# Kernel optimization log

Measured on AMD Instinct MI355X. Metric: run time of the kernel, lower is better.

The kernel has to match this reference:

```python
import jax, jax.numpy as jnp
import numpy as np


def lstm(x, W, U, b):
    """Keras LSTM with activation='relu', recurrent_activation='sigmoid'.
    x: [B, S, E]; W: [E, 4u]; U: [u, 4u]; b: [4u]. Gate order i,f,c,o.
    Returns (all hidden states [B,S,u], last hidden [B,u])."""
    B = x.shape[0]
    u = U.shape[0]
    h0 = jnp.zeros((B, u), x.dtype)
    c0 = jnp.zeros((B, u), x.dtype)

    def step(carry, xt):
        h, c = carry
        z = xt @ W + h @ U + b
        i, f, g, o = jnp.split(z, 4, axis=-1)
        i = jax.nn.sigmoid(i)
        f = jax.nn.sigmoid(f)
        g = jax.nn.relu(g)          # candidate activation = relu
        o = jax.nn.sigmoid(o)
        c = f * c + i * g
        h = o * jax.nn.relu(c)      # output activation = relu
        return (h, c), h

    (hT, _), hs = jax.lax.scan(step, (h0, c0), jnp.swapaxes(x, 0, 1))
    return jnp.swapaxes(hs, 0, 1), hT


def setup_inputs() -> dict:
    key = jax.random.key(0)
    ks = iter(jax.random.split(key, 64))

    def W(*s):
        return jax.random.normal(next(ks), s, jnp.float32) * 0.05

    V = 32000
    inp = {
        "t": jax.random.randint(next(ks), (8, 16, 64), 0, V, jnp.int32),
        "p": jax.random.randint(next(ks), (8, 16, 512), 0, V, jnp.int32),
        "emb_t": W(V, 128),
        "emb_p": W(V, 256),
        # title LSTMs: 128 (return_seq) -> 64
        "tl0_W": W(128, 512), "tl0_U": W(128, 512), "tl0_b": jnp.zeros((512,), jnp.float32),
        "tl1_W": W(128, 256), "tl1_U": W(64, 256),  "tl1_b": jnp.zeros((256,), jnp.float32),
        # title dense: 128 relu, 64 relu, 32 linear
        "td0_W": W(64, 128),  "td0_b": jnp.zeros((128,), jnp.float32),
        "td1_W": W(128, 64),  "td1_b": jnp.zeros((64,), jnp.float32),
        "td2_W": W(64, 32),   "td2_b": jnp.zeros((32,), jnp.float32),
        # parag LSTMs: 256 (rs) -> 128 (rs) -> 64
        "pl0_W": W(256, 1024), "pl0_U": W(256, 1024), "pl0_b": jnp.zeros((1024,), jnp.float32),
        "pl1_W": W(256, 512),  "pl1_U": W(128, 512),  "pl1_b": jnp.zeros((512,), jnp.float32),
        "pl2_W": W(128, 256),  "pl2_U": W(64, 256),   "pl2_b": jnp.zeros((256,), jnp.float32),
        # parag dense: 128 relu, 64 relu, 32 linear
        "pd0_W": W(64, 128),  "pd0_b": jnp.zeros((128,), jnp.float32),
        "pd1_W": W(128, 64),  "pd1_b": jnp.zeros((64,), jnp.float32),
        "pd2_W": W(64, 32),   "pd2_b": jnp.zeros((32,), jnp.float32),
        # head: 256 relu, 128 relu, 64 relu, 32 sigmoid
        "L0_W": W(64, 256),  "L0_b": jnp.zeros((256,), jnp.float32),
        "L1_W": W(256, 128), "L1_b": jnp.zeros((128,), jnp.float32),
        "L2_W": W(128, 64),  "L2_b": jnp.zeros((64,), jnp.float32),
        "L3_W": W(64, 32),   "L3_b": jnp.zeros((32,), jnp.float32),
    }
    return inp


def reference(t, p, emb_t, emb_p,
              tl0_W, tl0_U, tl0_b, tl1_W, tl1_U, tl1_b,
              td0_W, td0_b, td1_W, td1_b, td2_W, td2_b,
              pl0_W, pl0_U, pl0_b, pl1_W, pl1_U, pl1_b, pl2_W, pl2_U, pl2_b,
              pd0_W, pd0_b, pd1_W, pd1_b, pd2_W, pd2_b,
              L0_W, L0_b, L1_W, L1_b, L2_W, L2_b, L3_W, L3_b):
    B, N, St = t.shape
    Sp = p.shape[2]

    # The original loops over B and map_fn over a singleton axis; the math is
    # identical to running the stacks on a flattened [B*N] recurrent batch.
    xt = emb_t[t.reshape(B * N, St)]              # [BN, St, 128]
    xt, _ = lstm(xt, tl0_W, tl0_U, tl0_b)         # [BN, St, 128]
    _, ht = lstm(xt, tl1_W, tl1_U, tl1_b)         # [BN, 64]
    ht = jax.nn.relu(ht @ td0_W + td0_b)
    ht = jax.nn.relu(ht @ td1_W + td1_b)
    ht = ht @ td2_W + td2_b                       # [BN, 32] (no activation)

    xp = emb_p[p.reshape(B * N, Sp)]              # [BN, Sp, 256]
    xp, _ = lstm(xp, pl0_W, pl0_U, pl0_b)
    xp, _ = lstm(xp, pl1_W, pl1_U, pl1_b)
    _, hp = lstm(xp, pl2_W, pl2_U, pl2_b)         # [BN, 64]
    hp = jax.nn.relu(hp @ pd0_W + pd0_b)
    hp = jax.nn.relu(hp @ pd1_W + pd1_b)
    hp = hp @ pd2_W + pd2_b                       # [BN, 32]

    feat = jnp.concatenate([ht, hp], axis=-1).reshape(B, N, 64)
    x = feat.mean(axis=1)                         # reduce_mean over axis=-2 (N)
    x = jax.nn.relu(x @ L0_W + L0_b)
    x = jax.nn.relu(x @ L1_W + L1_b)
    x = jax.nn.relu(x @ L2_W + L2_b)
    x = jax.nn.sigmoid(x @ L3_W + L3_b)           # [B, 32]
    return x
```

## Files before the change

kernel.cpp:

```cpp
#include <hip/hip_runtime.h>
#include <hip/hip_fp16.h>

typedef _Float16 f16;
typedef _Float16 f16x8 __attribute__((ext_vector_type(8)));
typedef float    f32x4 __attribute__((ext_vector_type(4)));
typedef unsigned short ushort;
typedef unsigned int uint;
typedef unsigned long long u64;

__device__ __forceinline__ float sigm(float x) { return 1.f / (1.f + __expf(-x)); }
__device__ __forceinline__ float reluf(float x) { return x > 0.f ? x : 0.f; }
__device__ __forceinline__ float h2f(ushort u) { return (float)__builtin_bit_cast(f16, u); }
__device__ __forceinline__ ushort f2h(float v) { return __builtin_bit_cast(ushort, (f16)v); }

#define LDRLX(p)    __hip_atomic_load((p), __ATOMIC_RELAXED, __HIP_MEMORY_SCOPE_AGENT)
#define STRLX(p, v) __hip_atomic_store((p), (v), __ATOMIC_RELAXED, __HIP_MEMORY_SCOPE_AGENT)
#define MFMA16(a, b, c) __builtin_amdgcn_mfma_f32_16x16x32_f16((a), (b), (c), 0, 0, 0)

__device__ __forceinline__ void poll_all(uint* p, uint need, bool act) {
  bool done = !act;
  while (true) {
    if (!done) done = (LDRLX(p) >= need);
    if (__all((int)done)) break;
    __builtin_amdgcn_s_sleep(1);
  }
}

__device__ __forceinline__ u64 ldr64(const u64* p) {
  return __hip_atomic_load(p, __ATOMIC_RELAXED, __HIP_MEMORY_SCOPE_AGENT);
}
__device__ __forceinline__ void str64(u64* p, u64 v) {
  __hip_atomic_store(p, v, __ATOMIC_RELAXED, __HIP_MEMORY_SCOPE_AGENT);
}

template <int NR>
__device__ __forceinline__ void poll_recs(const u64* const (&ra)[NR],
                                          const uint (&nd)[NR], u64 (&rv)[NR]) {
  bool ok[NR];
#pragma unroll
  for (int i = 0; i < NR; i++) ok[i] = (nd[i] == 0u);
  while (true) {
    bool all = true;
#pragma unroll
    for (int i = 0; i < NR; i++) if (!ok[i]) rv[i] = ldr64(ra[i]);
#pragma unroll
    for (int i = 0; i < NR; i++) if (!ok[i]) ok[i] = ((uint)(rv[i] >> 32) >= nd[i]);
#pragma unroll
    for (int i = 0; i < NR; i++) all &= ok[i];
    if (all) return;
    __builtin_amdgcn_s_sleep(1);
  }
}

template <int KF>
__global__ void pack_bsw(const float* __restrict__ B, f16* __restrict__ dst, int N) {
  int id = blockIdx.x * 256 + threadIdx.x;
  int total = KF * 32 * N;
  if (id >= total) return;
  int j  = id & 7;
  int L  = (id >> 3) & 63;
  int r  = id >> 9;
  int kf = r & (KF - 1);
  int c  = r / KF;
  int k  = kf * 32 + ((L >> 4) * 8) + j;
  int n  = c * 16 + (L & 15);
  dst[id] = (f16)B[k * N + n];
}

template <int Sx, int K, int KF, int N, int NC, int MODE>
__global__ __launch_bounds__(256) void gemm_xw(const int* __restrict__ tok,
                                               const float* __restrict__ emb,
                                               const f16* __restrict__ Bsw,
                                               const float* __restrict__ bias,
                                               f16* __restrict__ X) {
  __shared__ int tokLds[64];
  __shared__ f16x8 bLds[8 * 64];
  const int tid = threadIdx.x;
  const int blk = blockIdx.x;
  const int g  = (MODE == 0) ? (blk >> 7) : (blk >> 4);
  const int t0 = (MODE == 0) ? ((blk & 127) * 4) : ((blk & 15) * 4);
  if (tid < 64) {
    int wv = tid >> 4, rho = tid & 15;
    tokLds[tid] = tok[(g * 16 + rho) * Sx + t0 + wv];
  }
  __syncthreads();
  const int wave = tid >> 6, lane = tid & 63;
  const int quad = lane >> 4, l16 = lane & 15;

  f16x8 a[KF];
  {
    const float* arow = emb + (long)tokLds[wave * 16 + l16] * K + quad * 8;
#pragma unroll
    for (int kf = 0; kf < KF; kf++) {
      float4 v0 = *(const float4*)(arow + kf * 32);
      float4 v1 = *(const float4*)(arow + kf * 32 + 4);
      f16x8 tv;
      tv[0] = (f16)v0.x; tv[1] = (f16)v0.y; tv[2] = (f16)v0.z; tv[3] = (f16)v0.w;
      tv[4] = (f16)v1.x; tv[5] = (f16)v1.y; tv[6] = (f16)v1.z; tv[7] = (f16)v1.w;
      a[kf] = tv;
    }
  }
  const int t = t0 + wave;
  const f16x8* Bfrag = (const f16x8*)Bsw;
  for (int c = 0; c < NC; c++) {
    for (int i = tid; i < KF * 64; i += 256) bLds[i] = Bfrag[c * KF * 64 + i];
    __syncthreads();
    f32x4 acc = {0.f, 0.f, 0.f, 0.f};
#pragma unroll
    for (int kf = 0; kf < KF; kf++)
      acc = MFMA16(a[kf], bLds[kf * 64 + lane], acc);
    const int col = c * 16 + l16;
    const float bc = bias[col];
    uint2 pk;
    pk.x = (uint)f2h(acc[0] + bc) | ((uint)f2h(acc[1] + bc) << 16);
    pk.y = (uint)f2h(acc[2] + bc) | ((uint)f2h(acc[3] + bc) << 16);
    size_t base;
    if (MODE == 0) {
      int gm = col >> 8, u = col & 255;
      base = (((size_t)(g * 512 + t) * 4 + gm) * 4096) + u * 16 + quad * 4;
    } else {
      int gm = col >> 7, u = col & 127;
      base = (((size_t)(g * 64 + t) * 4 + gm) * 2048) + u * 16 + quad * 4;
    }
    *(uint2*)(X + base) = pk;
    __syncthreads();
  }
}

struct RP {
  const f16 *xp2, *xt2;
  const f16 *U0f, *W1f, *U1f, *W2f, *U2f, *U0tf, *W1tf, *U1tf;
  const float *pl1_b, *pl2_b, *tl1_b;
  const float *pd0W, *pd0b, *pd1W, *pd1b, *pd2W, *pd2b;
  const float *td0W, *td0b, *td1W, *td1b, *td2W, *td2b;
  u64 *h0r, *h1r, *h0tr;
  uint *cnt;
  float* feat;
};

__global__ __launch_bounds__(256, 1) void recur_pipe(RP A) {
  __shared__ __align__(16) char smem[147968];
  const int tid = threadIdx.x;
  const int w = tid >> 6, lane = tid & 63;
  const int quad = lane >> 4, l16 = lane & 15;
  const int blk = blockIdx.x;
  const int role = blk >> 3, g = blk & 7;
  uint* mytag = A.cnt + (role * 8 + g) * 16;

  if (role < 4) {
    const int bb = role;
    f16* wlds = (f16*)smem;
    f16* hb   = (f16*)(smem + 131072);
    {
      const uint4* U0q = (const uint4*)A.U0f;
      uint4* wq = (uint4*)wlds;
      for (int idx = tid; idx < 8192; idx += 256) {
        int gm = idx >> 11, r = idx & 2047, wv = r >> 9, kf = (r >> 6) & 7, ln = r & 63;
        wq[idx] = U0q[((gm * 16 + 4 * bb + wv) * 8 + kf) * 64 + ln];
      }
    }
    for (int idx = tid; idx < 4224; idx += 256) hb[idx] = (f16)0.f;
    float c0[4] = {0.f, 0.f, 0.f, 0.f};
    u64* ringg = A.h0r + (size_t)g * 16384;
    int pp[3]; { int q = 0; for (int p = 0; p < 4; p++) if (p != bb) pp[q++] = p; }
    const uint2* xq2 = (const uint2*)A.xp2;
    const f16x8* wv8 = (const f16x8*)wlds;
    const int myu = 64 * bb + 16 * w + l16;
    uint* bpp = A.cnt;
    if (lane < 4) bpp = A.cnt + ((4 + lane) * 8 + g) * 16;
    __syncthreads();

    for (int t = 0; t < 512; t++) {
      uint2 xv[4];
      {
        size_t xb = ((size_t)(g * 512 + t) * 4) * 1024 + (size_t)myu * 4 + quad;
#pragma unroll
        for (int gm = 0; gm < 4; gm++) xv[gm] = xq2[xb + (size_t)gm * 1024];
      }
      {
        bool act = (lane < 4) && (t > 0) && ((t & 3) == 0);
        uint need = t > 4 ? (uint)(t - 4) : 0u;
        poll_all(bpp, need, act);
      }
      {
        const u64* slotb = ringg + (size_t)((t + 7) & 7) * 2048;
        const u64* ra[6]; uint nd[6]; u64 rv[6];
#pragma unroll
        for (int q = 0; q < 3; q++) {
          const u64* rb = slotb + pp[q] * 512 + 2 * tid;
          ra[q * 2] = rb; ra[q * 2 + 1] = rb + 1;
          nd[q * 2] = nd[q * 2 + 1] = (t > 0) ? (uint)t : 0u;
        }
        poll_recs<6>(ra, nd, rv);
        if (t > 0) {
          f16* dst = hb + (t & 1) * 4224;
          const int ul = tid >> 2;
#pragma unroll
          for (int q = 0; q < 3; q++)
#pragma unroll
            for (int j = 0; j < 2; j++) {
              uint pay = (uint)rv[q * 2 + j];
              int r0 = ((tid & 3) * 2 + j) * 2;
              dst[r0 * 264 + pp[q] * 64 + ul] = __builtin_bit_cast(f16, (ushort)pay);
              dst[(r0 + 1) * 264 + pp[q] * 64 + ul] = __builtin_bit_cast(f16, (ushort)(pay >> 16));
            }
        }
      }
      __syncthreads();
      f16x8 af[8];
#pragma unroll
      for (int kf = 0; kf < 8; kf++)
        af[kf] = *(const f16x8*)&hb[(t & 1) * 4224 + l16 * 264 + kf * 32 + quad * 8];
      f32x4 z[4];
#pragma unroll
      for (int gm = 0; gm < 4; gm++) {
        f32x4 zz = {0.f, 0.f, 0.f, 0.f};
#pragma unroll
        for (int kf = 0; kf < 8; kf++)
          zz = MFMA16(af[kf], wv8[((gm * 4 + w) * 8 + kf) * 64 + lane], zz);
        z[gm] = zz;
      }
      u64 xs[4];
#pragma unroll
      for (int gm = 0; gm < 4; gm++) xs[gm] = ((u64)xv[gm].y << 32) | xv[gm].x;
      ushort hs[4];
      f16* wbuf = hb + ((t + 1) & 1) * 4224;
#pragma unroll
      for (int r = 0; r < 4; r++) {
        float gi = sigm(z[0][r] + h2f((ushort)(xs[0] >> (16 * r))));
        float ff = sigm(z[1][r] + h2f((ushort)(xs[1] >> (16 * r))));
        float gg = reluf(z[2][r] + h2f((ushort)(xs[2] >> (16 * r))));
        float oo = sigm(z[3][r] + h2f((ushort)(xs[3] >> (16 * r))));
        c0[r] = ff * c0[r] + gi * gg;
        hs[r] = f2h(oo * reluf(c0[r]));
        wbuf[(quad * 4 + r) * 264 + myu] = __builtin_bit_cast(f16, hs[r]);
      }
      {
        u64 tg = ((u64)(uint)(t + 1)) << 32;
        u64* wb = ringg + (size_t)(t & 7) * 2048 + bb * 512 + (16 * w + l16) * 8 + quad * 2;
        str64(wb,     tg | (u64)((uint)hs[0] | ((uint)hs[1] << 16)));
        str64(wb + 1, tg | (u64)((uint)hs[2] | ((uint)hs[3] << 16)));
      }
    }
  } else if (role < 8) {
    const int bn = role - 4;
    f16* wlds = (f16*)smem;
    f16* h0c  = (f16*)(smem + 98304);
    f16* h1b  = (f16*)(smem + 106752);
    float* zL = (float*)(smem + 115456);
    {
      const uint4* W1q = (const uint4*)A.W1f;
      const uint4* U1q = (const uint4*)A.U1f;
      uint4* wq = (uint4*)wlds;
      for (int idx = tid; idx < 4096; idx += 256) {
        int gm = idx >> 10, r = idx & 1023, j2 = r >> 9, kf = (r >> 6) & 7, ln = r & 63;
        wq[idx] = W1q[((gm * 8 + bn * 2 + j2) * 8 + kf) * 64 + ln];
      }
      for (int idx = tid; idx < 2048; idx += 256) {
        int gm = idx >> 9, r = idx & 511, j2 = r >> 8, kf = (r >> 6) & 3, ln = r & 63;
        wq[4096 + idx] = U1q[((gm * 8 + bn * 2 + j2) * 4 + kf) * 64 + ln];
      }
    }
    for (int idx = tid; idx < 2176; idx += 256) h1b[idx] = (f16)0.f;
    float c1[2] = {0.f, 0.f};
    float bth[4];
    { int un = tid & 31; for (int gm = 0; gm < 4; gm++) bth[gm] = A.pl1_b[gm * 128 + 32 * bn + un]; }
    u64* h0rg = A.h0r + (size_t)g * 16384;
    u64* h1rg = A.h1r + (size_t)g * 8192;
    int pp[3]; { int q = 0; for (int p = 0; p < 4; p++) if (p != bn) pp[q++] = p; }
    const f16x8* wv8 = (const f16x8*)wlds;
    uint* bpp = A.cnt + (8 * 8 + g) * 16;
    __syncthreads();

    for (int t = 0; t < 512; t++) {
      {
        bool act = (lane == 0) && ((t & 3) == 0);
        uint need = t > 4 ? (uint)(t - 4) : 0u;
        poll_all(bpp, need, act);
      }
      const u64* ra[11]; uint nd[11]; u64 rv[11];
      {
        const u64* s0b = h0rg + (size_t)(t & 7) * 2048;
#pragma unroll
        for (int e = 0; e < 8; e++) { ra[e] = s0b + tid + 256 * e; nd[e] = (uint)(t + 1); }
        const u64* s1b = h1rg + (size_t)((t + 7) & 7) * 1024;
#pragma unroll
        for (int q = 0; q < 3; q++) { ra[8 + q] = s1b + pp[q] * 256 + tid; nd[8 + q] = (t > 0) ? (uint)t : 0u; }
      }
      poll_recs<11>(ra, nd, rv);
      {
#pragma unroll
        for (int e = 0; e < 8; e++) {
          int idx = tid + 256 * e;
          int q = idx >> 9, rr = idx & 511, uls = rr >> 3, rp = rr & 7;
          uint pay = (uint)rv[e];
          h0c[(2 * rp) * 264 + q * 64 + uls]     = __builtin_bit_cast(f16, (ushort)pay);
          h0c[(2 * rp + 1) * 264 + q * 64 + uls] = __builtin_bit_cast(f16, (ushort)(pay >> 16));
        }
        if (t > 0) {
          f16* dst = h1b + (t & 1) * 2176;
          int un = tid >> 3, sq = tid & 7;
#pragma unroll
          for (int q = 0; q < 3; q++) {
            uint pay = (uint)rv[8 + q];
            dst[sq * 136 + pp[q] * 32 + un]       = __builtin_bit_cast(f16, (ushort)pay);
            dst[(sq + 8) * 136 + pp[q] * 32 + un] = __builtin_bit_cast(f16, (ushort)(pay >> 16));
          }
        }
      }
      __syncthreads();
      if (tid == 0) STRLX(mytag, (uint)(t + 1));
      f16x8 af0[8], af1[4];
#pragma unroll
      for (int kf = 0; kf < 8; kf++)
        af0[kf] = *(const f16x8*)&h0c[l16 * 264 + kf * 32 + quad * 8];
#pragma unroll
      for (int kf = 0; kf < 4; kf++)
        af1[kf] = *(const f16x8*)&h1b[(t & 1) * 2176 + l16 * 136 + kf * 32 + quad * 8];
#pragma unroll
      for (int j2 = 0; j2 < 2; j2++) {
        f32x4 zz = {0.f, 0.f, 0.f, 0.f};
#pragma unroll
        for (int kf = 0; kf < 8; kf++)
          zz = MFMA16(af0[kf], wv8[((w * 2 + j2) * 8 + kf) * 64 + lane], zz);
#pragma unroll
        for (int kf = 0; kf < 4; kf++)
          zz = MFMA16(af1[kf], wv8[4096 + ((w * 2 + j2) * 4 + kf) * 64 + lane], zz);
#pragma unroll
        for (int r = 0; r < 4; r++)
          zL[(quad * 4 + r) * 132 + w * 32 + j2 * 16 + l16] = zz[r];
      }
      __syncthreads();
      {
        int sq = tid >> 5, un = tid & 31;
        f16* dst = h1b + ((t + 1) & 1) * 2176;
        ushort hh[2];
#pragma unroll
        for (int e = 0; e < 2; e++) {
          int s = sq + 8 * e;
          float gi = sigm(zL[s * 132 + un] + bth[0]);
          float ff = sigm(zL[s * 132 + 32 + un] + bth[1]);
          float gg = reluf(zL[s * 132 + 64 + un] + bth[2]);
          float oo = sigm(zL[s * 132 + 96 + un] + bth[3]);
          c1[e] = ff * c1[e] + gi * gg;
          float hv = oo * reluf(c1[e]);
          hh[e] = f2h(hv);
          dst[s * 136 + 32 * bn + un] = __builtin_bit_cast(f16, hh[e]);
        }
        u64 tg = ((u64)(uint)(t + 1)) << 32;
        str64(h1rg + (size_t)(t & 7) * 1024 + bn * 256 + un * 8 + sq,
              tg | (u64)((uint)hh[0] | ((uint)hh[1] << 16)));
      }
    }
  } else if (role == 8) {
    f16* wlds = (f16*)smem;
    f16* h1c  = (f16*)(smem + 98304);
    f16* h2db = (f16*)(smem + 107008);
    {
      const uint4* W2q = (const uint4*)A.W2f;
      const uint4* U2q = (const uint4*)A.U2f;
      uint4* wq = (uint4*)wlds;
      for (int idx = tid; idx < 4096; idx += 256) wq[idx] = W2q[idx];
      for (int idx = tid; idx < 2048; idx += 256) wq[4096 + idx] = U2q[idx];
    }
    for (int idx = tid; idx < 1152; idx += 256) h2db[idx] = (f16)0.f;
    float c2[4] = {0.f, 0.f, 0.f, 0.f};
    float b2[4];
#pragma unroll
    for (int gm = 0; gm < 4; gm++) b2[gm] = A.pl2_b[gm * 64 + 16 * w + l16];
    u64* h1rg = A.h1r + (size_t)g * 8192;
    const f16x8* wv8 = (const f16x8*)wlds;
    __syncthreads();

    for (int t = 0; t < 512; t++) {
      const u64* ra[4]; uint nd[4]; u64 rv[4];
      {
        const u64* s1b = h1rg + (size_t)(t & 7) * 1024;
#pragma unroll
        for (int e = 0; e < 4; e++) { ra[e] = s1b + tid + 256 * e; nd[e] = (uint)(t + 1); }
      }
      poll_recs<4>(ra, nd, rv);
      {
        f16* dst = h1c + (t & 1) * 2176;
#pragma unroll
        for (int e = 0; e < 4; e++) {
          int idx = tid + 256 * e;
          int bq = idx >> 8, rr = idx & 255, un = rr >> 3, sq = rr & 7;
          uint pay = (uint)rv[e];
          dst[sq * 136 + bq * 32 + un]       = __builtin_bit_cast(f16, (ushort)pay);
          dst[(sq + 8) * 136 + bq * 32 + un] = __builtin_bit_cast(f16, (ushort)(pay >> 16));
        }
      }
      __syncthreads();
      if (tid == 0) STRLX(mytag, (uint)(t + 1));
      f16x8 af0[4], af1[2];
#pragma unroll
      for (int kf = 0; kf < 4; kf++)
        af0[kf] = *(const f16x8*)&h1c[(t & 1) * 2176 + l16 * 136 + kf * 32 + quad * 8];
#pragma unroll
      for (int kf = 0; kf < 2; kf++)
        af1[kf] = *(const f16x8*)&h2db[(t & 1) * 1152 + l16 * 72 + kf * 32 + quad * 8];
      f32x4 z[4];
#pragma unroll
      for (int gm = 0; gm < 4; gm++) {
        f32x4 zz = {0.f, 0.f, 0.f, 0.f};
#pragma unroll
        for (int kf = 0; kf < 4; kf++)
          zz = MFMA16(af0[kf], wv8[((gm * 4 + w) * 4 + kf) * 64 + lane], zz);
#pragma unroll
        for (int kf = 0; kf < 2; kf++)
          zz = MFMA16(af1[kf], wv8[4096 + ((gm * 4 + w) * 2 + kf) * 64 + lane], zz);
        z[gm] = zz;
      }
#pragma unroll
      for (int r = 0; r < 4; r++) {
        float gi = sigm(z[0][r] + b2[0]);
        float ff = sigm(z[1][r] + b2[1]);
        float gg = reluf(z[2][r] + b2[2]);
        float oo = sigm(z[3][r] + b2[3]);
        c2[r] = ff * c2[r] + gi * gg;
        h2db[((t + 1) & 1) * 1152 + (quad * 4 + r) * 72 + 16 * w + l16] = (f16)(oo * reluf(c2[r]));
      }
    }
    __syncthreads();
    float* zmA = (float*)smem;
    float* zmB = (float*)(smem + 8448);
    const f16* hf = h2db;
#pragma unroll 1
    for (int e = 0; e < 8; e++) {
      const int idx = tid + 256 * e, sq = idx >> 7, j = idx & 127;
      float a = A.pd0b[j];
      for (int k = 0; k < 64; k++) a += (float)hf[sq * 72 + k] * A.pd0W[k * 128 + j];
      zmA[sq * 132 + j] = reluf(a);
    }
    __syncthreads();
#pragma unroll 1
    for (int e = 0; e < 4; e++) {
      const int idx = tid + 256 * e, sq = idx >> 6, j = idx & 63;
      float a = A.pd1b[j];
      for (int k = 0; k < 128; k++) a += zmA[sq * 132 + k] * A.pd1W[k * 64 + j];
      zmB[sq * 68 + j] = reluf(a);
    }
    __syncthreads();
#pragma unroll 1
    for (int e = 0; e < 2; e++) {
      const int idx = tid + 256 * e, sq = idx >> 5, j = idx & 31;
      float a = A.pd2b[j];
      for (int k = 0; k < 64; k++) a += zmB[sq * 68 + k] * A.pd2W[k * 32 + j];
      A.feat[(g * 16 + sq) * 64 + 32 + j] = a;
    }
  } else if (role < 11) {
    const int bb = role - 9;
    f16* wlds = (f16*)smem;
    f16* hb   = (f16*)(smem + 65536);
    {
      const uint4* U0tq = (const uint4*)A.U0tf;
      uint4* wq = (uint4*)wlds;
      for (int idx = tid; idx < 4096; idx += 256) {
        int gm = idx >> 10, r = idx & 1023, wv = r >> 8, kf = (r >> 6) & 3, ln = r & 63;
        wq[idx] = U0tq[((gm * 8 + 4 * bb + wv) * 4 + kf) * 64 + ln];
      }
    }
    for (int idx = tid; idx < 2176; idx += 256) hb[idx] = (f16)0.f;
    float c0[4] = {0.f, 0.f, 0.f, 0.f};
    u64* ringg = A.h0tr + (size_t)g * 8192;
    const uint2* xq2 = (const uint2*)A.xt2;
    const f16x8* wv8 = (const f16x8*)wlds;
    const int myu = 64 * bb + 16 * w + l16;
    const int pbb = bb ^ 1;
    uint* bpp = A.cnt + (11 * 8 + g) * 16;
    __syncthreads();

    for (int t = 0; t < 64; t++) {
      uint2 xv[4];
      {
        size_t xb = ((size_t)(g * 64 + t) * 4) * 512 + (size_t)myu * 4 + quad;
#pragma unroll
        for (int gm = 0; gm < 4; gm++) xv[gm] = xq2[xb + (size_t)gm * 512];
      }
      {
        bool act = (lane == 0) && (t > 0) && ((t & 3) == 0);
        uint need = t > 4 ? (uint)(t - 4) : 0u;
        poll_all(bpp, need, act);
      }
      {
        const u64* ra[2]; uint nd[2]; u64 rv[2];
        const u64* rb = ringg + (size_t)((t + 7) & 7) * 1024 + pbb * 512 + 2 * tid;
        ra[0] = rb; ra[1] = rb + 1;
        nd[0] = nd[1] = (t > 0) ? (uint)t : 0u;
        poll_recs<2>(ra, nd, rv);
        if (t > 0) {
          f16* dst = hb + (t & 1) * 2176;
          const int ul = tid >> 2;
#pragma unroll
          for (int j = 0; j < 2; j++) {
            uint pay = (uint)rv[j];
            int r0 = ((tid & 3) * 2 + j) * 2;
            dst[r0 * 136 + pbb * 64 + ul]       = __builtin_bit_cast(f16, (ushort)pay);
            dst[(r0 + 1) * 136 + pbb * 64 + ul] = __builtin_bit_cast(f16, (ushort)(pay >> 16));
          }
        }
      }
      __syncthreads();
      f16x8 af[4];
#pragma unroll
      for (int kf = 0; kf < 4; kf++)
        af[kf] = *(const f16x8*)&hb[(t & 1) * 2176 + l16 * 136 + kf * 32 + quad * 8];
      f32x4 z[4];
#pragma unroll
      for (int gm = 0; gm < 4; gm++) {
        f32x4 zz = {0.f, 0.f, 0.f, 0.f};
#pragma unroll
        for (int kf = 0; kf < 4; kf++)
          zz = MFMA16(af[kf], wv8[((gm * 4 + w) * 4 + kf) * 64 + lane], zz);
        z[gm] = zz;
      }
      u64 xs[4];
#pragma unroll
      for (int gm = 0; gm < 4; gm++) xs[gm] = ((u64)xv[gm].y << 32) | xv[gm].x;
      ushort hs[4];
      f16* wbuf = hb + ((t + 1) & 1) * 2176;
#pragma unroll
      for (int r = 0; r < 4; r++) {
        float gi = sigm(z[0][r] + h2f((ushort)(xs[0] >> (16 * r))));
        float ff = sigm(z[1][r] + h2f((ushort)(xs[1] >> (16 * r))));
        float gg = reluf(z[2][r] + h2f((ushort)(xs[2] >> (16 * r))));
        float oo = sigm(z[3][r] + h2f((ushort)(xs[3] >> (16 * r))));
        c0[r] = ff * c0[r] + gi * gg;
        hs[r] = f2h(oo * reluf(c0[r]));
        wbuf[(quad * 4 + r) * 136 + myu] = __builtin_bit_cast(f16, hs[r]);
      }
      {
        u64 tg = ((u64)(uint)(t + 1)) << 32;
        u64* wb = ringg + (size_t)(t & 7) * 1024 + bb * 512 + (16 * w + l16) * 8 + quad * 2;
        str64(wb,     tg | (u64)((uint)hs[0] | ((uint)hs[1] << 16)));
        str64(wb + 1, tg | (u64)((uint)hs[2] | ((uint)hs[3] << 16)));
      }
    }
  } else {
    f16* wlds = (f16*)smem;
    f16* h0tc = (f16*)(smem + 98304);
    f16* h1db = (f16*)(smem + 107008);
    {
      const uint4* W1tq = (const uint4*)A.W1tf;
      const uint4* U1tq = (const uint4*)A.U1tf;
      uint4* wq = (uint4*)wlds;
      for (int idx = tid; idx < 4096; idx += 256) wq[idx] = W1tq[idx];
      for (int idx = tid; idx < 2048; idx += 256) wq[4096 + idx] = U1tq[idx];
    }
    for (int idx = tid; idx < 1152; idx += 256) h1db[idx] = (f16)0.f;
    float c1[4] = {0.f, 0.f, 0.f, 0.f};
    float bt[4];
#pragma unroll
    for (int gm = 0; gm < 4; gm++) bt[gm] = A.tl1_b[gm * 64 + 16 * w + l16];
    u64* ringg = A.h0tr + (size_t)g * 8192;
    const f16x8* wv8 = (const f16x8*)wlds;
    __syncthreads();

    for (int t = 0; t < 64; t++) {
      const u64* ra[4]; uint nd[4]; u64 rv[4];
      {
        const u64* base = ringg + (size_t)(t & 7) * 1024;
#pragma unroll
        for (int e = 0; e < 4; e++) { ra[e] = base + tid + 256 * e; nd[e] = (uint)(t + 1); }
      }
      poll_recs<4>(ra, nd, rv);
      {
        f16* dst = h0tc + (t & 1) * 2176;
#pragma unroll
        for (int e = 0; e < 4; e++) {
          int idx = tid + 256 * e;
          int q = idx >> 9, rr = idx & 511, uls = rr >> 3, rp = rr & 7;
          uint pay = (uint)rv[e];
          dst[(2 * rp) * 136 + q * 64 + uls]     = __builtin_bit_cast(f16, (ushort)pay);
          dst[(2 * rp + 1) * 136 + q * 64 + uls] = __builtin_bit_cast(f16, (ushort)(pay >> 16));
        }
      }
      __syncthreads();
      if (tid == 0) STRLX(mytag, (uint)(t + 1));
      f16x8 af0[4], af1[2];
#pragma unroll
      for (int kf = 0; kf < 4; kf++)
        af0[kf] = *(const f16x8*)&h0tc[(t & 1) * 2176 + l16 * 136 + kf * 32 + quad * 8];
#pragma unroll
      for (int kf = 0; kf < 2; kf++)
        af1[kf] = *(const f16x8*)&h1db[(t & 1) * 1152 + l16 * 72 + kf * 32 + quad * 8];
      f32x4 z[4];
#pragma unroll
      for (int gm = 0; gm < 4; gm++) {
        f32x4 zz = {0.f, 0.f, 0.f, 0.f};
#pragma unroll
        for (int kf = 0; kf < 4; kf++)
          zz = MFMA16(af0[kf], wv8[((gm * 4 + w) * 4 + kf) * 64 + lane], zz);
#pragma unroll
        for (int kf = 0; kf < 2; kf++)
          zz = MFMA16(af1[kf], wv8[4096 + ((gm * 4 + w) * 2 + kf) * 64 + lane], zz);
        z[gm] = zz;
      }
#pragma unroll
      for (int r = 0; r < 4; r++) {
        float gi = sigm(z[0][r] + bt[0]);
        float ff = sigm(z[1][r] + bt[1]);
        float gg = reluf(z[2][r] + bt[2]);
        float oo = sigm(z[3][r] + bt[3]);
        c1[r] = ff * c1[r] + gi * gg;
        h1db[((t + 1) & 1) * 1152 + (quad * 4 + r) * 72 + 16 * w + l16] = (f16)(oo * reluf(c1[r]));
      }
    }
    __syncthreads();
    float* zmA = (float*)smem;
    float* zmB = (float*)(smem + 8448);
    const f16* hf = h1db;
#pragma unroll 1
    for (int e = 0; e < 8; e++) {
      const int idx = tid + 256 * e, sq = idx >> 7, j = idx & 127;
      float a = A.td0b[j];
      for (int k = 0; k < 64; k++) a += (float)hf[sq * 72 + k] * A.td0W[k * 128 + j];
      zmA[sq * 132 + j] = reluf(a);
    }
    __syncthreads();
#pragma unroll 1
    for (int e = 0; e < 4; e++) {
      const int idx = tid + 256 * e, sq = idx >> 6, j = idx & 63;
      float a = A.td1b[j];
      for (int k = 0; k < 128; k++) a += zmA[sq * 132 + k] * A.td1W[k * 64 + j];
      zmB[sq * 68 + j] = reluf(a);
    }
    __syncthreads();
#pragma unroll 1
    for (int e = 0; e < 2; e++) {
      const int idx = tid + 256 * e, sq = idx >> 5, j = idx & 31;
      float a = A.td2b[j];
      for (int k = 0; k < 64; k++) a += zmB[sq * 68 + k] * A.td2W[k * 32 + j];
      A.feat[(g * 16 + sq) * 64 + j] = a;
    }
  }
}

__global__ __launch_bounds__(256) void head_kernel(const float* __restrict__ feat,
    const float* __restrict__ L0W, const float* __restrict__ L0b,
    const float* __restrict__ L1W, const float* __restrict__ L1b,
    const float* __restrict__ L2W, const float* __restrict__ L2b,
    const float* __restrict__ L3W, const float* __restrict__ L3b,
    float* __restrict__ out) {
  __shared__ float xb[512];
  __shared__ float y0[2048];
  __shared__ float y1[1024];
  __shared__ float y2[512];
  const int tid = threadIdx.x;
  for (int idx = tid; idx < 512; idx += 256) {
    int b = idx >> 6, d = idx & 63;
    float s = 0.f;
    for (int n = 0; n < 16; n++) s += feat[(b * 16 + n) * 64 + d];
    xb[idx] = s * (1.f / 16.f);
  }
  __syncthreads();
  for (int idx = tid; idx < 2048; idx += 256) {
    int b = idx >> 8, j = idx & 255;
    float a = L0b[j];
    for (int k = 0; k < 64; k++) a += xb[b * 64 + k] * L0W[k * 256 + j];
    y0[idx] = reluf(a);
  }
  __syncthreads();
  for (int idx = tid; idx < 1024; idx += 256) {
    int b = idx >> 7, j = idx & 127;
    float a = L1b[j];
    for (int k = 0; k < 256; k++) a += y0[b * 256 + k] * L1W[k * 128 + j];
    y1[idx] = reluf(a);
  }
  __syncthreads();
  for (int idx = tid; idx < 512; idx += 256) {
    int b = idx >> 6, j = idx & 63;
    float a = L2b[j];
    for (int k = 0; k < 128; k++) a += y1[b * 128 + k] * L2W[k * 64 + j];
    y2[idx] = reluf(a);
  }
  __syncthreads();
  {
    int b = tid >> 5, j = tid & 31;
    float a = L3b[j];
    for (int k = 0; k < 64; k++) a += y2[b * 64 + k] * L3W[k * 32 + j];
    out[b * 32 + j] = 1.f / (1.f + __expf(-a));
  }
}

extern "C" void kernel_launch(void* const* d_in, const int* in_sizes, int n_in,
                              void* d_out, int out_size, void* d_ws, size_t ws_size,
                              hipStream_t stream) {
  const int*   t_tok = (const int*)d_in[0];
  const int*   p_tok = (const int*)d_in[1];
  const float* emb_t = (const float*)d_in[2];
  const float* emb_p = (const float*)d_in[3];
  const float* tl0_W = (const float*)d_in[4];
  const float* tl0_U = (const float*)d_in[5];
  const float* tl0_b = (const float*)d_in[6];
  const float* tl1_W = (const float*)d_in[7];
  const float* tl1_U = (const float*)d_in[8];
  const float* tl1_b = (const float*)d_in[9];
  const float* td0_W = (const float*)d_in[10];
  const float* td0_b = (const float*)d_in[11];
  const float* td1_W = (const float*)d_in[12];
  const float* td1_b = (const float*)d_in[13];
  const float* td2_W = (const float*)d_in[14];
  const float* td2_b = (const float*)d_in[15];
  const float* pl0_W = (const float*)d_in[16];
  const float* pl0_U = (const float*)d_in[17];
  const float* pl0_b = (const float*)d_in[18];
  const float* pl1_W = (const float*)d_in[19];
  const float* pl1_U = (const float*)d_in[20];
  const float* pl1_b = (const float*)d_in[21];
  const float* pl2_W = (const float*)d_in[22];
  const float* pl2_U = (const float*)d_in[23];
  const float* pl2_b = (const float*)d_in[24];
  const float* pd0_W = (const float*)d_in[25];
  const float* pd0_b = (const float*)d_in[26];
  const float* pd1_W = (const float*)d_in[27];
  const float* pd1_b = (const float*)d_in[28];
  const float* pd2_W = (const float*)d_in[29];
  const float* pd2_b = (const float*)d_in[30];
  const float* L0_W  = (const float*)d_in[31];
  const float* L0_b  = (const float*)d_in[32];
  const float* L1_W  = (const float*)d_in[33];
  const float* L1_b  = (const float*)d_in[34];
  const float* L2_W  = (const float*)d_in[35];
  const float* L2_b  = (const float*)d_in[36];
  const float* L3_W  = (const float*)d_in[37];
  const float* L3_b  = (const float*)d_in[38];

  char* ws = (char*)d_ws;
  size_t off = 0;
  auto alloc = [&](size_t bytes) {
    void* ptr = ws + off;
    off += (bytes + 255) & ~(size_t)255;
    return ptr;
  };
  f16* xp2  = (f16*)alloc((size_t)8 * 512 * 4 * 4096 * 2);
  f16* xt2  = (f16*)alloc((size_t)8 * 64 * 4 * 2048 * 2);
  f16* Bp   = (f16*)alloc((size_t)256 * 1024 * 2);
  f16* Bt   = (f16*)alloc((size_t)128 * 512 * 2);
  f16* U0f  = (f16*)alloc((size_t)256 * 1024 * 2);
  f16* W1f  = (f16*)alloc((size_t)256 * 512 * 2);
  f16* U1f  = (f16*)alloc((size_t)128 * 512 * 2);
  f16* W2f  = (f16*)alloc((size_t)128 * 256 * 2);
  f16* U2f  = (f16*)alloc((size_t)64 * 256 * 2);
  f16* U0tf = (f16*)alloc((size_t)128 * 512 * 2);
  f16* W1tf = (f16*)alloc((size_t)128 * 256 * 2);
  f16* U1tf = (f16*)alloc((size_t)64 * 256 * 2);
  size_t ringoff = off;
  u64* h0r  = (u64*)alloc((size_t)8 * 16384 * 8);
  u64* h1r  = (u64*)alloc((size_t)8 * 8192 * 8);
  u64* h0tr = (u64*)alloc((size_t)8 * 8192 * 8);
  uint* cnt = (uint*)alloc((size_t)96 * 16 * 4);
  size_t ringlen = off - ringoff;
  float* feat = (float*)alloc((size_t)128 * 64 * 4);

  hipMemsetAsync(ws + ringoff, 0, ringlen, stream);

  pack_bsw<8><<<1024, 256, 0, stream>>>(pl0_W, Bp, 1024);
  pack_bsw<4><<<256, 256, 0, stream>>>(tl0_W, Bt, 512);
  pack_bsw<8><<<1024, 256, 0, stream>>>(pl0_U, U0f, 1024);
  pack_bsw<8><<<512, 256, 0, stream>>>(pl1_W, W1f, 512);
  pack_bsw<4><<<256, 256, 0, stream>>>(pl1_U, U1f, 512);
  pack_bsw<4><<<128, 256, 0, stream>>>(pl2_W, W2f, 256);
  pack_bsw<2><<<64, 256, 0, stream>>>(pl2_U, U2f, 256);
  pack_bsw<4><<<256, 256, 0, stream>>>(tl0_U, U0tf, 512);
  pack_bsw<4><<<128, 256, 0, stream>>>(tl1_W, W1tf, 256);
  pack_bsw<2><<<64, 256, 0, stream>>>(tl1_U, U1tf, 256);
  gemm_xw<512, 256, 8, 1024, 64, 0><<<1024, 256, 0, stream>>>(p_tok, emb_p, Bp, pl0_b, xp2);
  gemm_xw<64, 128, 4, 512, 32, 1><<<128, 256, 0, stream>>>(t_tok, emb_t, Bt, tl0_b, xt2);

  RP ra;
  ra.xp2 = xp2; ra.xt2 = xt2;
  ra.U0f = U0f; ra.W1f = W1f; ra.U1f = U1f; ra.W2f = W2f; ra.U2f = U2f;
  ra.U0tf = U0tf; ra.W1tf = W1tf; ra.U1tf = U1tf;
  ra.pl1_b = pl1_b; ra.pl2_b = pl2_b; ra.tl1_b = tl1_b;
  ra.pd0W = pd0_W; ra.pd0b = pd0_b; ra.pd1W = pd1_W; ra.pd1b = pd1_b;
  ra.pd2W = pd2_W; ra.pd2b = pd2_b;
  ra.td0W = td0_W; ra.td0b = td0_b; ra.td1W = td1_W; ra.td1b = td1_b;
  ra.td2W = td2_W; ra.td2b = td2_b;
  ra.h0r = h0r; ra.h1r = h1r; ra.h0tr = h0tr; ra.cnt = cnt;
  ra.feat = feat;
  recur_pipe<<<96, 256, 0, stream>>>(ra);

  head_kernel<<<1, 256, 0, stream>>>(feat, L0_W, L0_b, L1_W, L1_b, L2_W, L2_b,
                                     L3_W, L3_b, (float*)d_out);
}
```

Baseline: 1.508 ms.

## Remap ring buffer records for coalesced access and use lightweight LDS barriers

Changes the layout of the hidden-state ring records that producer blocks write and consumer blocks read, so that consecutive threads touch consecutive slots in global memory and in LDS. Replaces __syncthreads with a barrier that waits only on LDS counters (lgkmcnt) and not on outstanding global stores. This targets per-step latency in the serial recurrence. It adds an extra barrier at the end of the layer-1 step, and it risks ordering bugs if any global writes must complete before the barrier.

```diff
diff --git a/kernel.cpp b/kernel.cpp
--- a/kernel.cpp
+++ b/kernel.cpp
@@ -16,6 +16,8 @@
 #define LDRLX(p)    __hip_atomic_load((p), __ATOMIC_RELAXED, __HIP_MEMORY_SCOPE_AGENT)
 #define STRLX(p, v) __hip_atomic_store((p), (v), __ATOMIC_RELAXED, __HIP_MEMORY_SCOPE_AGENT)
 #define MFMA16(a, b, c) __builtin_amdgcn_mfma_f32_16x16x32_f16((a), (b), (c), 0, 0, 0)
+#define LBAR() do { asm volatile("s_waitcnt lgkmcnt(0)" ::: "memory"); \
+                    __builtin_amdgcn_s_barrier(); } while (0)
 
 __device__ __forceinline__ void poll_all(uint* p, uint need, bool act) {
   bool done = !act;
@@ -166,6 +168,8 @@
     const uint2* xq2 = (const uint2*)A.xp2;
     const f16x8* wv8 = (const f16x8*)wlds;
     const int myu = 64 * bb + 16 * w + l16;
+    const int ulq = 16 * ((tid >> 4) & 3) + (tid & 15);
+    const int qd  = tid >> 6;
     uint* bpp = A.cnt;
     if (lane < 4) bpp = A.cnt + ((4 + lane) * 8 + g) * 16;
     __syncthreads();
@@ -194,19 +198,18 @@
         poll_recs<6>(ra, nd, rv);
         if (t > 0) {
           f16* dst = hb + (t & 1) * 4224;
-          const int ul = tid >> 2;
 #pragma unroll
           for (int q = 0; q < 3; q++)
 #pragma unroll
             for (int j = 0; j < 2; j++) {
               uint pay = (uint)rv[q * 2 + j];
-              int r0 = ((tid & 3) * 2 + j) * 2;
-              dst[r0 * 264 + pp[q] * 64 + ul] = __builtin_bit_cast(f16, (ushort)pay);
-              dst[(r0 + 1) * 264 + pp[q] * 64 + ul] = __builtin_bit_cast(f16, (ushort)(pay >> 16));
+              int r0 = qd * 4 + 2 * j;
+              dst[r0 * 264 + pp[q] * 64 + ulq]       = __builtin_bit_cast(f16, (ushort)pay);
+              dst[(r0 + 1) * 264 + pp[q] * 64 + ulq] = __builtin_bit_cast(f16, (ushort)(pay >> 16));
             }
         }
       }
-      __syncthreads();
+      LBAR();
       f16x8 af[8];
 #pragma unroll
       for (int kf = 0; kf < 8; kf++)
@@ -237,7 +240,8 @@
       }
       {
         u64 tg = ((u64)(uint)(t + 1)) << 32;
-        u64* wb = ringg + (size_t)(t & 7) * 2048 + bb * 512 + (16 * w + l16) * 8 + quad * 2;
+        u64* wb = ringg + (size_t)(t & 7) * 2048 + bb * 512 +
+                  quad * 128 + w * 32 + l16 * 2;
         str64(wb,     tg | (u64)((uint)hs[0] | ((uint)hs[1] << 16)));
         str64(wb + 1, tg | (u64)((uint)hs[2] | ((uint)hs[3] << 16)));
       }
@@ -292,23 +296,26 @@
 #pragma unroll
         for (int e = 0; e < 8; e++) {
           int idx = tid + 256 * e;
-          int q = idx >> 9, rr = idx & 511, uls = rr >> 3, rp = rr & 7;
+          int bbq = idx >> 9, r = idx & 511;
+          int jj = r & 1, l16c = (r >> 1) & 15, wc = (r >> 5) & 3, qdc = (r >> 7) & 3;
+          int col = bbq * 64 + 16 * wc + l16c;
+          int r0 = qdc * 4 + 2 * jj;
           uint pay = (uint)rv[e];
-          h0c[(2 * rp) * 264 + q * 64 + uls]     = __builtin_bit_cast(f16, (ushort)pay);
-          h0c[(2 * rp + 1) * 264 + q * 64 + uls] = __builtin_bit_cast(f16, (ushort)(pay >> 16));
+          h0c[r0 * 264 + col]       = __builtin_bit_cast(f16, (ushort)pay);
+          h0c[(r0 + 1) * 264 + col] = __builtin_bit_cast(f16, (ushort)(pay >> 16));
         }
         if (t > 0) {
           f16* dst = h1b + (t & 1) * 2176;
-          int un = tid >> 3, sq = tid & 7;
+          int sqc = tid >> 5, unc = tid & 31;
 #pragma unroll
           for (int q = 0; q < 3; q++) {
             uint pay = (uint)rv[8 + q];
-            dst[sq * 136 + pp[q] * 32 + un]       = __builtin_bit_cast(f16, (ushort)pay);
-            dst[(sq + 8) * 136 + pp[q] * 32 + un] = __builtin_bit_cast(f16, (ushort)(pay >> 16));
+            dst[sqc * 136 + pp[q] * 32 + unc]       = __builtin_bit_cast(f16, (ushort)pay);
+            dst[(sqc + 8) * 136 + pp[q] * 32 + unc] = __builtin_bit_cast(f16, (ushort)(pay >> 16));
           }
         }
       }
-      __syncthreads();
+      LBAR();
       if (tid == 0) STRLX(mytag, (uint)(t + 1));
       f16x8 af0[8], af1[4];
 #pragma unroll
@@ -330,7 +337,7 @@
         for (int r = 0; r < 4; r++)
           zL[(quad * 4 + r) * 132 + w * 32 + j2 * 16 + l16] = zz[r];
       }
-      __syncthreads();
+      LBAR();
       {
         int sq = tid >> 5, un = tid & 31;
         f16* dst = h1b + ((t + 1) & 1) * 2176;
@@ -348,9 +355,10 @@
           dst[s * 136 + 32 * bn + un] = __builtin_bit_cast(f16, hh[e]);
         }
         u64 tg = ((u64)(uint)(t + 1)) << 32;
-        str64(h1rg + (size_t)(t & 7) * 1024 + bn * 256 + un * 8 + sq,
+        str64(h1rg + (size_t)(t & 7) * 1024 + bn * 256 + tid,
               tg | (u64)((uint)hh[0] | ((uint)hh[1] << 16)));
       }
+      LBAR();
     }
   } else if (role == 8) {
     f16* wlds = (f16*)smem;
@@ -385,13 +393,14 @@
 #pragma unroll
         for (int e = 0; e < 4; e++) {
           int idx = tid + 256 * e;
-          int bq = idx >> 8, rr = idx & 255, un = rr >> 3, sq = rr & 7;
+          int bq = idx >> 8, r = idx & 255;
+          int sqc = r >> 5, unc = r & 31;
           uint pay = (uint)rv[e];
-          dst[sq * 136 + bq * 32 + un]       = __builtin_bit_cast(f16, (ushort)pay);
-          dst[(sq + 8) * 136 + bq * 32 + un] = __builtin_bit_cast(f16, (ushort)(pay >> 16));
+          dst[sqc * 136 + bq * 32 + unc]       = __builtin_bit_cast(f16, (ushort)pay);
+          dst[(sqc + 8) * 136 + bq * 32 + unc] = __builtin_bit_cast(f16, (ushort)(pay >> 16));
         }
       }
-      __syncthreads();
+      LBAR();
       if (tid == 0) STRLX(mytag, (uint)(t + 1));
       f16x8 af0[4], af1[2];
 #pragma unroll
@@ -501,7 +510,7 @@
           }
         }
       }
-      __syncthreads();
+      LBAR();
       f16x8 af[4];
 #pragma unroll
       for (int kf = 0; kf < 4; kf++)
@@ -576,7 +585,7 @@
           dst[(2 * rp + 1) * 136 + q * 64 + uls] = __builtin_bit_cast(f16, (ushort)(pay >> 16));
         }
       }
-      __syncthreads();
+      LBAR();
       if (tid == 0) STRLX(mytag, (uint)(t + 1));
       f16x8 af0[4], af1[2];
 #pragma unroll
```

New measurement: 1.455 ms. -3.5%, faster.
